# Kernel optimization log

Hardware: AMD Instinct MI355X
Metric: run time of the kernel (lower is better)

## Reference

```python
import jax, jax.numpy as jnp
import numpy as np

KH, KW = 2, 2
GRID_SIZE = 5
SPLINE_ORDER = 3
IN_FEATURES = KH * KW
N_COEF = GRID_SIZE + SPLINE_ORDER  # 8
N_KNOTS = GRID_SIZE + 2 * SPLINE_ORDER + 1  # 12


def b_splines(x, grid, spline_order):
    """x: (N, in), grid: (in, n_knots) -> (N, in, grid_size + spline_order).
    Cox-de-Boor recursion, identical to efficient-kan's b_splines."""
    x_ = x[..., None]  # (N, in, 1)
    bases = ((x_ >= grid[:, :-1]) & (x_ < grid[:, 1:])).astype(x.dtype)
    for k in range(1, spline_order + 1):
        left = (x_ - grid[:, : -(k + 1)]) / (grid[:, k:-1] - grid[:, : -(k + 1)])
        right = (grid[:, k + 1:] - x_) / (grid[:, k + 1:] - grid[:, 1:-k])
        bases = left * bases[..., :-1] + right * bases[..., 1:]
    return bases  # (N, in, N_COEF)


def setup_inputs() -> dict:
    key = jax.random.key(0)
    k1, k2, k3, k4 = jax.random.split(key, 4)
    B, C, H, W = 8, 16, 128, 128
    x = jax.random.normal(k1, (B, C, H, W), dtype=jnp.float32) * 0.5  # mostly inside grid_range
    base_weight = jax.random.normal(k2, (1, IN_FEATURES), dtype=jnp.float32) * 0.5
    spline_weight = jax.random.normal(k3, (1, IN_FEATURES, N_COEF), dtype=jnp.float32) * 0.1
    spline_scaler = 1.0 + jax.random.normal(k4, (1, IN_FEATURES), dtype=jnp.float32) * 0.1
    # uniform extended knot grid over grid_range=[-1, 1], same per input feature (buffer)
    h = 2.0 / GRID_SIZE
    g = np.arange(-SPLINE_ORDER, GRID_SIZE + SPLINE_ORDER + 1, dtype=np.float32) * h - 1.0
    grid = jnp.asarray(np.broadcast_to(g, (IN_FEATURES, N_KNOTS)).copy())
    return {"x": x, "base_weight": base_weight, "spline_weight": spline_weight,
            "spline_scaler": spline_scaler, "grid": grid}


def reference(x, base_weight, spline_weight, spline_scaler, grid):
    B, C, H, W = x.shape
    Ho, Wo = H - KH + 1, W - KW + 1  # stride 1, no padding, no dilation
    # unfold: (B, C, Ho, Wo, KH*KW), window elements in torch Unfold row-major order
    patches = jnp.stack([x[:, :, i:i + Ho, j:j + Wo]
                         for i in range(KH) for j in range(KW)], axis=-1)
    flat = patches.reshape(-1, IN_FEATURES)  # (N, 4)
    # KANLinear: base path (SiLU activation then linear)
    base = jax.nn.silu(flat) @ base_weight.T  # (N, 1)
    # spline path
    bas = b_splines(flat, grid, SPLINE_ORDER)  # (N, 4, 8)
    sw = spline_weight * spline_scaler[..., None]  # scaled_spline_weight (1, 4, 8)
    spline = bas.reshape(flat.shape[0], -1) @ sw.reshape(sw.shape[0], -1).T  # (N, 1)
    out = (base + spline).reshape(B, C, Ho, Wo)
    # multiple_convs_kan_conv2d accumulates the per-channel results into one output channel
    return out.sum(axis=1, keepdims=True)  # (B, 1, Ho, Wo)
```

## Files before the change

kernel.cpp:

```cpp
#include <hip/hip_runtime.h>


#define IN_F 4
#define N_COEF 8
#define N_INT 11
#define TW 32
#define TH 8
#define LW 33
#define LH 9
#define NV (LW * LH)
#define CG 4

__device__ __forceinline__ float silu(float x) {
    return x * __builtin_amdgcn_rcpf(1.0f + __expf(-x));
}

__global__ __launch_bounds__(256) void kan_conv_kernel(
    const float* __restrict__ x,
    const float* __restrict__ base_w,
    const float* __restrict__ spline_w,
    const float* __restrict__ spline_s,
    const float* __restrict__ grid,
    float* __restrict__ out,
    int B, int C, int H, int W)
{
    const int Ho = H - 1, Wo = W - 1;

    __shared__ float4 coef[N_INT][IN_F];
    __shared__ float  sfeat[IN_F][NV];
    __shared__ float  s_misc[6];

    const int tid = threadIdx.x;

    if (tid < N_INT * IN_F) {
        const int t = tid / IN_F;
        const int p = tid % IN_F;
        const float M[4][4] = {
            {1.f/6.f, -3.f/6.f,  3.f/6.f, -1.f/6.f},
            {4.f/6.f,  0.f,     -6.f/6.f,  3.f/6.f},
            {1.f/6.f,  3.f/6.f,  3.f/6.f, -3.f/6.f},
            {0.f,      0.f,      0.f,      1.f/6.f}};
        const float scal = spline_s[p];
        float c0 = 0.f, c1 = 0.f, c2 = 0.f, c3 = 0.f;
        #pragma unroll
        for (int m = 0; m < 4; ++m) {
            const int j = t - 3 + m;
            const float w = (j >= 0 && j < N_COEF)
                              ? spline_w[p * N_COEF + j] * scal : 0.f;
            c0 += M[m][0] * w; c1 += M[m][1] * w;
            c2 += M[m][2] * w; c3 += M[m][3] * w;
        }
        coef[t][p] = make_float4(c0, c1, c2, c3);
    }
    if (tid < IN_F) s_misc[tid] = base_w[tid];
    if (tid == 4)   s_misc[4] = grid[0];
    if (tid == 5)   s_misc[5] = 1.0f / (grid[1] - grid[0]);

    int bid = blockIdx.x;
    const int cg  = bid & 3;  bid >>= 2;
    const int txi = bid & 3;  bid >>= 2;
    const int tyi = bid & 15; bid >>= 4;
    const int b   = bid;
    const int tx0 = txi * TW, ty0 = tyi * TH, c0ch = cg * CG;

    const int lx = tid & (TW - 1);
    const int ly = tid >> 5;
    const int oy = ty0 + ly, ox = tx0 + lx;

    __syncthreads();
    const float bw0 = s_misc[0], bw1 = s_misc[1];
    const float bw2 = s_misc[2], bw3 = s_misc[3];
    const float g0 = s_misc[4], invh = s_misc[5];
    const float bw[4] = {bw0, bw1, bw2, bw3};

    float acc = 0.f;

    #pragma unroll
    for (int g = 0; g < CG; ++g) {
        const int c = c0ch + g;
        const float* __restrict__ xc = x + ((size_t)(b * C + c) * H) * W;

        if (g > 0) __syncthreads();

        #pragma unroll
        for (int v = tid; v < NV; v += 256) {
            const int r  = v / LW;
            const int cc = v - r * LW;
            const int iy = ty0 + r, ix = tx0 + cc;
            const float val = (iy < H && ix < W) ? xc[iy * W + ix] : 0.f;

            const float sil = silu(val);
            const float tf  = (val - g0) * invh;
            const float tfl = floorf(tf);
            const int   ti  = (int)tfl;
            const float u   = tf - tfl;
            const bool  valid = ((unsigned)ti < (unsigned)N_INT);
            const int   tc  = valid ? ti : 0;

            #pragma unroll
            for (int p = 0; p < IN_F; ++p) {
                const float4 cf = coef[tc][p];
                float sp = fmaf(u, cf.w, cf.z);
                sp = fmaf(u, sp, cf.y);
                sp = fmaf(u, sp, cf.x);
                sfeat[p][v] = fmaf(sil, bw[p], valid ? sp : 0.f);
            }
        }
        __syncthreads();

        const int i00 = ly * LW + lx;
        acc += sfeat[0][i00] + sfeat[1][i00 + 1]
             + sfeat[2][i00 + LW] + sfeat[3][i00 + LW + 1];
    }

    if (oy < Ho && ox < Wo)
        atomicAdd(&out[((size_t)b * Ho + oy) * Wo + ox], acc);
}

extern "C" void kernel_launch(void* const* d_in, const int* in_sizes, int n_in,
                              void* d_out, int out_size, void* d_ws, size_t ws_size,
                              hipStream_t stream) {
    const float* x        = (const float*)d_in[0];
    const float* base_w   = (const float*)d_in[1];
    const float* spline_w = (const float*)d_in[2];
    const float* spline_s = (const float*)d_in[3];
    const float* grid     = (const float*)d_in[4];
    float* out = (float*)d_out;

    const int B = 8, C = 16, H = 128, W = 128;

    hipMemsetAsync(out, 0, (size_t)out_size * sizeof(float), stream);

    kan_conv_kernel<<<2048, 256, 0, stream>>>(
        x, base_w, spline_w, spline_s, grid, out, B, C, H, W);
}
```

Measured before the change: 75.08 us.

## Reduce all channels per block in registers and drop atomics and memset

Each block now processes all 16 input channels for its tile, with one thread per halo pixel. Each thread accumulates the per-feature spline and SiLU terms across channels in registers, so the 2x2 window sum is done once per tile instead of once per channel. This removes the per-channel barriers, the atomicAdd output accumulation and the separate memset launch. In exchange there are fewer blocks (512) of 320 threads, and each thread holds 16 loaded values in registers, which could reduce occupancy.

```diff
diff --git a/kernel.cpp b/kernel.cpp
--- a/kernel.cpp
+++ b/kernel.cpp
@@ -9,13 +9,14 @@
 #define LW 33
 #define LH 9
 #define NV (LW * LH)
-#define CG 4
+#define NC 16
+#define NT 320
 
-__device__ __forceinline__ float silu(float x) {
+__device__ __forceinline__ float silu_f(float x) {
     return x * __builtin_amdgcn_rcpf(1.0f + __expf(-x));
 }
 
-__global__ __launch_bounds__(256) void kan_conv_kernel(
+__global__ __launch_bounds__(NT) void kan_conv_kernel(
     const float* __restrict__ x,
     const float* __restrict__ base_w,
     const float* __restrict__ spline_w,
@@ -26,15 +27,15 @@
 {
     const int Ho = H - 1, Wo = W - 1;
 
-    __shared__ float4 coef[N_INT][IN_F];
-    __shared__ float  sfeat[IN_F][NV];
+    __shared__ float4 coef[N_INT][IN_F + 1];
+    __shared__ float  sfeat[IN_F][NV + 7];
     __shared__ float  s_misc[6];
 
     const int tid = threadIdx.x;
 
     if (tid < N_INT * IN_F) {
-        const int t = tid / IN_F;
-        const int p = tid % IN_F;
+        const int t = tid >> 2;
+        const int p = tid & 3;
         const float M[4][4] = {
             {1.f/6.f, -3.f/6.f,  3.f/6.f, -1.f/6.f},
             {4.f/6.f,  0.f,     -6.f/6.f,  3.f/6.f},
@@ -57,64 +58,72 @@
     if (tid == 5)   s_misc[5] = 1.0f / (grid[1] - grid[0]);
 
     int bid = blockIdx.x;
-    const int cg  = bid & 3;  bid >>= 2;
     const int txi = bid & 3;  bid >>= 2;
     const int tyi = bid & 15; bid >>= 4;
     const int b   = bid;
-    const int tx0 = txi * TW, ty0 = tyi * TH, c0ch = cg * CG;
-
-    const int lx = tid & (TW - 1);
-    const int ly = tid >> 5;
-    const int oy = ty0 + ly, ox = tx0 + lx;
+    const int tx0 = txi * TW, ty0 = tyi * TH;
 
     __syncthreads();
-    const float bw0 = s_misc[0], bw1 = s_misc[1];
-    const float bw2 = s_misc[2], bw3 = s_misc[3];
+
     const float g0 = s_misc[4], invh = s_misc[5];
-    const float bw[4] = {bw0, bw1, bw2, bw3};
 
-    float acc = 0.f;
+    if (tid < NV) {
+        const int r  = tid / LW;
+        const int cc = tid - r * LW;
+        const int iy = ty0 + r, ix = tx0 + cc;
+        const bool inb = (iy < H) & (ix < W);
+        const size_t cs = (size_t)H * W;
+        const float* __restrict__ px =
+            x + (size_t)b * C * cs + (inb ? (iy * W + ix) : 0);
 
-    #pragma unroll
-    for (int g = 0; g < CG; ++g) {
-        const int c = c0ch + g;
-        const float* __restrict__ xc = x + ((size_t)(b * C + c) * H) * W;
+        float vals[NC];
+        #pragma unroll
+        for (int c = 0; c < NC; ++c) vals[c] = px[c * cs];
 
-        if (g > 0) __syncthreads();
-
+        float a0 = 0.f, a1 = 0.f, a2 = 0.f, a3 = 0.f, ssum = 0.f;
         #pragma unroll
-        for (int v = tid; v < NV; v += 256) {
-            const int r  = v / LW;
-            const int cc = v - r * LW;
-            const int iy = ty0 + r, ix = tx0 + cc;
-            const float val = (iy < H && ix < W) ? xc[iy * W + ix] : 0.f;
-
-            const float sil = silu(val);
+        for (int c = 0; c < NC; ++c) {
+            const float val = inb ? vals[c] : 0.f;
+            ssum += silu_f(val);
             const float tf  = (val - g0) * invh;
             const float tfl = floorf(tf);
             const int   ti  = (int)tfl;
             const float u   = tf - tfl;
             const bool  valid = ((unsigned)ti < (unsigned)N_INT);
             const int   tc  = valid ? ti : 0;
-
-            #pragma unroll
-            for (int p = 0; p < IN_F; ++p) {
-                const float4 cf = coef[tc][p];
-                float sp = fmaf(u, cf.w, cf.z);
-                sp = fmaf(u, sp, cf.y);
-                sp = fmaf(u, sp, cf.x);
-                sfeat[p][v] = fmaf(sil, bw[p], valid ? sp : 0.f);
-            }
+            const float4 f0 = coef[tc][0];
+            const float4 f1 = coef[tc][1];
+            const float4 f2 = coef[tc][2];
+            const float4 f3 = coef[tc][3];
+            float s0 = fmaf(u, f0.w, f0.z); s0 = fmaf(u, s0, f0.y); s0 = fmaf(u, s0, f0.x);
+            float s1 = fmaf(u, f1.w, f1.z); s1 = fmaf(u, s1, f1.y); s1 = fmaf(u, s1, f1.x);
+            float s2 = fmaf(u, f2.w, f2.z); s2 = fmaf(u, s2, f2.y); s2 = fmaf(u, s2, f2.x);
+            float s3 = fmaf(u, f3.w, f3.z); s3 = fmaf(u, s3, f3.y); s3 = fmaf(u, s3, f3.x);
+            a0 += valid ? s0 : 0.f;
+            a1 += valid ? s1 : 0.f;
+            a2 += valid ? s2 : 0.f;
+            a3 += valid ? s3 : 0.f;
         }
-        __syncthreads();
-
-        const int i00 = ly * LW + lx;
-        acc += sfeat[0][i00] + sfeat[1][i00 + 1]
-             + sfeat[2][i00 + LW] + sfeat[3][i00 + LW + 1];
+        const float bw0 = s_misc[0], bw1 = s_misc[1];
+        const float bw2 = s_misc[2], bw3 = s_misc[3];
+        sfeat[0][tid] = fmaf(ssum, bw0, a0);
+        sfeat[1][tid] = fmaf(ssum, bw1, a1);
+        sfeat[2][tid] = fmaf(ssum, bw2, a2);
+        sfeat[3][tid] = fmaf(ssum, bw3, a3);
     }
 
-    if (oy < Ho && ox < Wo)
-        atomicAdd(&out[((size_t)b * Ho + oy) * Wo + ox], acc);
+    __syncthreads();
+
+    if (tid < TW * TH) {
+        const int lx = tid & (TW - 1);
+        const int ly = tid >> 5;
+        const int oy = ty0 + ly, ox = tx0 + lx;
+        const int i00 = ly * LW + lx;
+        const float acc = sfeat[0][i00] + sfeat[1][i00 + 1]
+                        + sfeat[2][i00 + LW] + sfeat[3][i00 + LW + 1];
+        if (oy < Ho && ox < Wo)
+            out[((size_t)b * Ho + oy) * Wo + ox] = acc;
+    }
 }
 
 extern "C" void kernel_launch(void* const* d_in, const int* in_sizes, int n_in,
@@ -129,8 +138,6 @@
 
     const int B = 8, C = 16, H = 128, W = 128;
 
-    hipMemsetAsync(out, 0, (size_t)out_size * sizeof(float), stream);
-
-    kan_conv_kernel<<<2048, 256, 0, stream>>>(
+    kan_conv_kernel<<<512, NT, 0, stream>>>(
         x, base_w, spline_w, spline_s, grid, out, B, C, H, W);
 }
```

Result: faster. 69.97 us (-6.8%).
